# Optimization experiments

Measured on AMD Instinct MI355X. Metric: run time of the kernel, lower is better.

Reference implementation:

```python
import jax, jax.numpy as jnp
import numpy as np

V, D, H = 50000, 256, 4
HD = H * D            # concat head dim (TransformerConv concat=True)
HH, O = 256, 256      # invariant_hidden_dim, invariant_out_dim
B, N, E, L, A = 16, 1000, 4000, 64, 128
PAD = 0
SCALE = 1.0 / float(np.sqrt(D))


def emb_lookup(table, idx):
    # nn.Embedding with padding_idx: forward is a plain gather; grad at pad row is zeroed.
    rows = table[idx]
    return jnp.where((idx == PAD)[..., None], jax.lax.stop_gradient(rows), rows)


def transformer_conv(x, edge_index, ea, Wq, bq, Wk, bk, Wv, bv, We, Wskip, bskip):
    # PyG TransformerConv, heads=H, concat=True, root_weight=True, beta=False, dropout=0 (eval)
    n = x.shape[0]
    src, dst = edge_index[0], edge_index[1]
    q = (x @ Wq + bq).reshape(n, H, D)
    e = (ea @ We).reshape(-1, H, D)          # lin_edge (bias=False)
    k = (x @ Wk + bk).reshape(n, H, D)[src] + e
    v = (x @ Wv + bv).reshape(n, H, D)[src] + e
    alpha = (q[dst] * k).sum(-1) * SCALE      # [E,H]
    amax = jax.ops.segment_max(alpha, dst, num_segments=n)
    ex = jnp.exp(alpha - amax[dst])
    denom = jax.ops.segment_sum(ex, dst, num_segments=n)
    w = ex / denom[dst]                       # per-target-node softmax over incoming edges
    agg = jax.ops.segment_sum(v * w[..., None], dst, num_segments=n)
    return agg.reshape(n, HD) + x @ Wskip + bskip  # lin_skip on root


def mixed_embed(tok, node, graph_repr, emb):
    fixed = emb_lookup(emb, tok)
    flex = jnp.take_along_axis(graph_repr, node[..., None], axis=1)
    flex = jnp.where((node == PAD)[..., None], jax.lax.stop_gradient(flex), flex)
    return fixed + flex


def gru_last(xs, W_ih, W_hh, b_ih, b_hh):
    # torch nn.GRU, batch_first, 1 layer; only last hidden state is used
    gx = jnp.einsum('blh,gh->blg', xs, W_ih) + b_ih  # [B,L,3O]

    def step(h, g):
        gh = h @ W_hh.T + b_hh
        xr, xz, xn = jnp.split(g, 3, axis=-1)
        hr, hz, hn = jnp.split(gh, 3, axis=-1)
        r = jax.nn.sigmoid(xr + hr)
        z = jax.nn.sigmoid(xz + hz)
        c = jnp.tanh(xn + r * hn)
        return (1.0 - z) * c + z * h, None

    h0 = jnp.zeros((xs.shape[0], W_hh.shape[1]), xs.dtype)
    h_last, _ = jax.lax.scan(step, h0, jnp.swapaxes(gx, 0, 1))
    return h_last


def setup_inputs() -> dict:
    key = jax.random.key(0)
    ks = jax.random.split(key, 40)
    f = lambda i, shape, s=0.05: jax.random.normal(ks[i], shape, jnp.float32) * s
    ri = lambda i, shape, hi: jax.random.randint(ks[i], shape, 0, hi)
    return {
        'node_tokens': ri(0, (B, N), V),
        'edge_tokens': ri(1, (B, E), V),
        'edge_index': ri(2, (B, 2, E), N),
        'inv_token': ri(3, (B, L), V),
        'inv_node': ri(4, (B, L), N),
        'aa_token': ri(5, (B, A), V),
        'aa_node': ri(6, (B, A), N),
        'action_mask': jnp.ones((B, A), jnp.float32),
        'emb': f(7, (V, D), 0.02),
        'Wq': f(8, (D, HD)), 'bq': f(9, (HD,)),
        'Wk': f(10, (D, HD)), 'bk': f(11, (HD,)),
        'Wv': f(12, (D, HD)), 'bv': f(13, (HD,)),
        'We': f(14, (D, HD)),
        'Wskip': f(15, (D, HD)), 'bskip': f(16, (HD,)),
        'W1': f(17, (HD, D)), 'b1': f(18, (D,)),
        'Wp': f(19, (D, HH)), 'bp': f(20, (HH,)),
        'W_ih': f(21, (3 * O, HH)), 'W_hh': f(22, (3 * O, O)),
        'b_ih': f(23, (3 * O,)), 'b_hh': f(24, (3 * O,)),
        'Wab': f(25, (D, 1)), 'bab': f(26, (1,)),
        'Wap': f(27, (D, O)), 'bap': f(28, (O,)),
    }


def reference(node_tokens, edge_tokens, edge_index, inv_token, inv_node, aa_token, aa_node,
              action_mask, emb, Wq, bq, Wk, bk, Wv, bv, We, Wskip, bskip, W1, b1,
              Wp, bp, W_ih, W_hh, b_ih, b_hh, Wab, bab, Wap, bap):
    x = emb_lookup(emb, node_tokens)    # [B,N,D]
    ea = emb_lookup(emb, edge_tokens)   # [B,E,D]
    conv = jax.vmap(lambda xx, ei, ee: transformer_conv(
        xx, ei, ee, Wq, bq, Wk, bk, Wv, bv, We, Wskip, bskip))
    h = jax.nn.relu(conv(x, edge_index, ea))            # [B,N,HD]
    graph_repr = jax.nn.relu(h @ W1 + b1)               # [B,N,D]
    inv_h = jax.nn.relu(mixed_embed(inv_token, inv_node, graph_repr, emb) @ Wp + bp)
    inv = gru_last(inv_h, W_ih, W_hh, b_ih, b_hh)       # [B,O]
    aa_emb = mixed_embed(aa_token, aa_node, graph_repr, emb)  # [B,A,D]
    scores = jnp.einsum('bao,bo->ba', aa_emb @ Wap + bap, inv) + (aa_emb @ Wab + bab)[..., 0]
    inf_mask = jnp.maximum(jnp.log(action_mask), jnp.float32(np.finfo(np.float32).min))
    return scores + inf_mask
```

## Files before the change

kernel.cpp:

```cpp
#include <hip/hip_runtime.h>
#include <hip/hip_bf16.h>
#include <float.h>
#include <math.h>

typedef __hip_bfloat16 bf16;

#define B_ 16
#define N_ 1000
#define E_ 4000
#define L_ 64
#define A_ 128
#define D_ 256
#define H_ 4
#define HD_ 1024
#define SCALE_ 0.0625f

typedef __attribute__((ext_vector_type(8))) short short8;
typedef __attribute__((ext_vector_type(4))) float f32x4;

union U4S8 { uint4 u; short8 s; };

__device__ __forceinline__ unsigned short f2bf(float f) {
    bf16 h = __float2bfloat16(f);
    return *reinterpret_cast<unsigned short*>(&h);
}
__device__ __forceinline__ unsigned pack2(float a, float b) {
    return (unsigned)f2bf(a) | ((unsigned)f2bf(b) << 16);
}
__device__ __forceinline__ unsigned short rne1(float a) {
    unsigned ua = __float_as_uint(a);
    ua += 0x7fff + ((ua >> 16) & 1);
    return (unsigned short)(ua >> 16);
}
__device__ __forceinline__ float bflo(unsigned u) { return __uint_as_float(u << 16); }
__device__ __forceinline__ float bfhi(unsigned u) { return __uint_as_float(u & 0xffff0000u); }

#define LOG2E 1.4426950408889634f
__device__ __forceinline__ float fsigm(float x) {
    return __builtin_amdgcn_rcpf(1.f + __builtin_amdgcn_exp2f(-LOG2E * x));
}
__device__ __forceinline__ float ftanh(float x) {
    return 1.f - 2.f * __builtin_amdgcn_rcpf(1.f + __builtin_amdgcn_exp2f(2.f * LOG2E * x));
}

typedef const __attribute__((address_space(1))) unsigned int* gas_t;
typedef __attribute__((address_space(3))) unsigned int* las_t;
__device__ __forceinline__ void gld16(const void* g, void* l) {
    __builtin_amdgcn_global_load_lds((gas_t)g, (las_t)l, 16, 0, 0);
}

__global__ void convemb_kernel(const float* __restrict__ src, bf16* __restrict__ dst, long n4)
{
    long i = (long)blockIdx.x * 256 + threadIdx.x;
    if (i >= n4) return;
    float4 v = *(const float4*)(src + i * 4);
    *(uint2*)(dst + i * 4) = make_uint2(pack2(v.x, v.y), pack2(v.z, v.w));
}

__global__ void pack_all_kernel(const float* __restrict__ Wq, const float* __restrict__ Wk,
                                const float* __restrict__ Wv, const float* __restrict__ Wskip,
                                const float* __restrict__ We, const float* __restrict__ W1,
                                const float* __restrict__ Wp, const float* __restrict__ W_ih,
                                const float* __restrict__ Wap, const float* __restrict__ W_hh,
                                const float* __restrict__ bq, const float* __restrict__ bk,
                                const float* __restrict__ bv, const float* __restrict__ bskip,
                                unsigned* __restrict__ qkvsP, unsigned* __restrict__ WeP,
                                unsigned* __restrict__ W1P, unsigned* __restrict__ WpP,
                                unsigned* __restrict__ WihP, unsigned* __restrict__ WapP,
                                unsigned* __restrict__ WeTP,
                                short8* __restrict__ WhhP, float* __restrict__ bias4096)
{
    int i = blockIdx.x * 256 + threadIdx.x;
    if (i < 524288) {
        int k2 = i >> 12, n = i & 4095;
        const float* s = (n < 1024) ? Wq : (n < 2048) ? Wk : (n < 3072) ? Wv : Wskip;
        int col = n & 1023;
        qkvsP[i] = pack2(s[(long)(2 * k2) * 1024 + col], s[(long)(2 * k2 + 1) * 1024 + col]);
        return;
    }
    i -= 524288;
    if (i < 131072) {
        int k2 = i >> 10, n = i & 1023;
        WeP[i] = pack2(We[(long)(2 * k2) * 1024 + n], We[(long)(2 * k2 + 1) * 1024 + n]);
        return;
    }
    i -= 131072;
    if (i < 131072) {
        int k2 = i >> 8, n = i & 255;
        W1P[i] = pack2(W1[(long)(2 * k2) * 256 + n], W1[(long)(2 * k2 + 1) * 256 + n]);
        return;
    }
    i -= 131072;
    if (i < 32768) {
        int k2 = i >> 8, n = i & 255;
        WpP[i] = pack2(Wp[(long)(2 * k2) * 256 + n], Wp[(long)(2 * k2 + 1) * 256 + n]);
        return;
    }
    i -= 32768;
    if (i < 98304) {
        int k2 = i / 768, n = i % 768;
        WihP[i] = pack2(W_ih[(long)n * 256 + 2 * k2], W_ih[(long)n * 256 + 2 * k2 + 1]);
        return;
    }
    i -= 98304;
    if (i < 32768) {
        int k2 = i >> 8, n = i & 255;
        WapP[i] = pack2(Wap[(long)(2 * k2) * 256 + n], Wap[(long)(2 * k2 + 1) * 256 + n]);
        return;
    }
    i -= 32768;
    if (i < 131072) {
        int k2 = i >> 10, n = i & 1023;
        int d = n & 255, hb = n & ~255;
        WeTP[i] = pack2(We[(long)d * 1024 + hb + 2 * k2],
                        We[(long)d * 1024 + hb + 2 * k2 + 1]);
        return;
    }
    i -= 131072;
    if (i < 24576) {
        int lane = i & 63, tk = (i >> 6) & 7, tile = i >> 9;
        int n = tile * 16 + (lane & 15);
        const float* wp = W_hh + (long)n * 256 + tk * 32 + (lane >> 4) * 8;
        float4 w0 = *(const float4*)wp;
        float4 w1 = *(const float4*)(wp + 4);
        U4S8 u;
        u.u = make_uint4(pack2(w0.x, w0.y), pack2(w0.z, w0.w),
                         pack2(w1.x, w1.y), pack2(w1.z, w1.w));
        WhhP[i] = u.s;
        return;
    }
    i -= 24576;
    if (i < 4096) {
        int q = i >> 10, c = i & 1023;
        bias4096[i] = ((q == 0) ? bq : (q == 1) ? bk : (q == 2) ? bv : bskip)[c];
    }
}
#define PACK_ALL_TOT (524288 + 131072 + 131072 + 32768 + 98304 + 32768 + 131072 + 24576 + 4096)

#define TM 128
#define TN 128
#define TK 32
#define BSTR 132

template <typename CT>
__global__ __launch_bounds__(256)
void pgemm_kernel(const bf16* __restrict__ A, const int* __restrict__ arows,
                  const unsigned* __restrict__ Bp, const float* __restrict__ bias,
                  CT* __restrict__ C, int M, int K, int Nc, int relu_out,
                  long astride, int aoff, int colbase, int hslice, int addC, int outT)
{
    __shared__ short    As[TM * TK];
    __shared__ unsigned Bs[(TK / 2) * BSTR];

    const int tid  = threadIdx.x;
    const int lane = tid & 63;
    const int wave = tid >> 6;
    const int wm = wave >> 1, wn = wave & 1;
    const int quad = lane >> 4, c16 = lane & 15;
    const long row0 = (long)blockIdx.y * TM;
    const int  col0 = colbase + blockIdx.x * TN;
    const int  aoff2 = aoff + (hslice ? (col0 & ~255) : 0);

    {
    }
    const int r0 = wave * 32 + (lane >> 2);
    const int cseg = (lane & 3) * 8;
    long gr0 = row0 + r0;      if (gr0 > M - 1) gr0 = M - 1;
    long gr1 = row0 + r0 + 16; if (gr1 > M - 1) gr1 = M - 1;
    long ar0 = arows ? (long)arows[gr0] : gr0;
    long ar1 = arows ? (long)arows[gr1] : gr1;
    const short* Ag0 = (const short*)A + ar0 * astride + aoff2 + cseg;
    const short* Ag1 = (const short*)A + ar1 * astride + aoff2 + cseg;
    short* Ld0 = &As[wave * 1024];
    short* Ld1 = &As[wave * 1024 + 512];

    const int sn2 = tid & 63;
    const int skk = wave * 4;

    f32x4 acc[4][4];
    #pragma unroll
    for (int i = 0; i < 4; ++i)
        #pragma unroll
        for (int j = 0; j < 4; ++j)
            acc[i][j] = (f32x4){0.f, 0.f, 0.f, 0.f};

    for (int k0 = 0; k0 < K; k0 += TK) {
        gld16(Ag0 + k0, Ld0);
        gld16(Ag1 + k0, Ld1);
        #pragma unroll
        for (int i = 0; i < 4; ++i) {
            int kk2 = skk + i;
            *(uint2*)&Bs[kk2 * BSTR + sn2 * 2] =
                *(const uint2*)&Bp[(long)(k0 / 2 + kk2) * Nc + col0 + sn2 * 2];
        }
        __syncthreads();

        short8 af[4];
        U4S8   bfr[4];
        #pragma unroll
        for (int mi = 0; mi < 4; ++mi) {
            int m = wm * 64 + mi * 16 + c16;
            af[mi] = *(const short8*)&As[m * 32 + quad * 8];
        }
        #pragma unroll
        for (int ni = 0; ni < 4; ++ni) {
            int n = wn * 64 + ni * 16 + c16;
            uint4 u;
            u.x = Bs[(quad * 4 + 0) * BSTR + n];
            u.y = Bs[(quad * 4 + 1) * BSTR + n];
            u.z = Bs[(quad * 4 + 2) * BSTR + n];
            u.w = Bs[(quad * 4 + 3) * BSTR + n];
            bfr[ni].u = u;
        }
        #pragma unroll
        for (int mi = 0; mi < 4; ++mi)
            #pragma unroll
            for (int ni = 0; ni < 4; ++ni)
                acc[mi][ni] = __builtin_amdgcn_mfma_f32_16x16x32_bf16(
                    af[mi], bfr[ni].s, acc[mi][ni], 0, 0, 0);
        __syncthreads();
    }

    #pragma unroll
    for (int ni = 0; ni < 4; ++ni) {
        int col = col0 + wn * 64 + ni * 16 + c16;
        float bv = bias ? bias[col] : 0.f;
        #pragma unroll
        for (int mi = 0; mi < 4; ++mi) {
            long row = row0 + wm * 64 + mi * 16 + quad * 4;
            #pragma unroll
            for (int r = 0; r < 4; ++r) {
                if (row + r >= M) continue;
                float v = acc[mi][ni][r] + bv;
                if (addC) v += (float)C[(row + r) * Nc + col];
                if (relu_out) v = fmaxf(v, 0.f);
                if (outT) {
                    long rr = row + r;
                    int t = (int)(rr & 63), b = (int)(rr >> 6);
                    C[((long)t * Nc + col) * 16 + b] = (CT)v;
                } else {
                    C[(row + r) * Nc + col] = (CT)v;
                }
            }
        }
    }
}

__global__ void zero_int_kernel(int* __restrict__ p, int n)
{
    int i = blockIdx.x * 256 + threadIdx.x;
    if (i < n) p[i] = 0;
}

__global__ void count_kernel(const int* __restrict__ edge_index, int b0,
                             int* __restrict__ cnt, int cE)
{
    int i = blockIdx.x * 256 + threadIdx.x;
    if (i >= cE) return;
    int bl = i / E_, ei = i % E_;
    int dst = edge_index[(long)(b0 + bl) * 2 * E_ + E_ + ei];
    atomicAdd(&cnt[bl * N_ + dst], 1);
}

__global__ __launch_bounds__(1024)
void scan_kernel(const int* __restrict__ cnt, int* __restrict__ row_start,
                 int* __restrict__ cursor)
{
    int bl = blockIdx.x;
    int tid = threadIdx.x;
    __shared__ int s[1024];
    int v = (tid < N_) ? cnt[bl * N_ + tid] : 0;
    s[tid] = v;
    __syncthreads();
    for (int off = 1; off < 1024; off <<= 1) {
        int t = (tid >= off) ? s[tid - off] : 0;
        __syncthreads();
        s[tid] += t;
        __syncthreads();
    }
    if (tid < N_) {
        int excl = s[tid] - v;
        row_start[bl * N_ + tid] = excl;
        cursor[bl * N_ + tid] = excl;
    }
}

__global__ void scatter_kernel(const int* __restrict__ edge_index, int b0,
                               int* __restrict__ cursor, int* __restrict__ elist, int cE)
{
    int i = blockIdx.x * 256 + threadIdx.x;
    if (i >= cE) return;
    int bl = i / E_, ei = i % E_;
    int dst = edge_index[(long)(b0 + bl) * 2 * E_ + E_ + ei];
    int pos = atomicAdd(&cursor[bl * N_ + dst], 1);
    elist[bl * E_ + pos] = ei;
}

__device__ __forceinline__ float d2(unsigned a, unsigned b)
{
    return bflo(a) * bflo(b) + bfhi(a) * bfhi(b);
}

__global__ void attn_kernel(const bf16* __restrict__ qkvs, const bf16* __restrict__ qWb,
                            const bf16* __restrict__ embh,
                            const int* __restrict__ edge_tokens, const int* __restrict__ edge_index,
                            const int* __restrict__ row_start, const int* __restrict__ cnt,
                            const int* __restrict__ elist, int b0,
                            bf16* __restrict__ aggb, bf16* __restrict__ xsumb)
{
    int base = blockIdx.x;
    int bl = base / N_;
    int tid = threadIdx.x;
    int l = tid & 63;
    int j0 = tid * 4;
    int jx = l * 4;

    uint2 qq = *(const uint2*)(qkvs + (long)base * 4096 + j0);
    uint2 ww = *(const uint2*)(qWb + (long)base * 1024 + j0);

    int start = row_start[base];
    int deg = cnt[base];
    const int* el = elist + (long)bl * E_;
    const int* srcp = edge_index + (long)(b0 + bl) * 2 * E_;
    const int* tokp = edge_tokens + (long)(b0 + bl) * E_;

    float denom = 0.f;
    float v0 = 0.f, v1 = 0.f, v2 = 0.f, v3 = 0.f;
    float x0 = 0.f, x1 = 0.f, x2 = 0.f, x3 = 0.f;

    for (int t = 0; t < deg; ++t) {
        int ei = el[start + t];
        int src = srcp[ei];
        int tok = tokp[ei];
        const bf16* srow = qkvs + (long)(bl * N_ + src) * 4096;
        uint2 kk = *(const uint2*)(srow + 1024 + j0);
        uint2 vv = *(const uint2*)(srow + 2048 + j0);
        uint2 xx = *(const uint2*)(embh + (long)tok * 256 + jx);

        float s = d2(qq.x, kk.x) + d2(qq.y, kk.y) + d2(ww.x, xx.x) + d2(ww.y, xx.y);
        s += __shfl_xor(s, 32);
        s += __shfl_xor(s, 16);
        s += __shfl_xor(s, 8);
        s += __shfl_xor(s, 4);
        s += __shfl_xor(s, 2);
        s += __shfl_xor(s, 1);
        float ex = __builtin_amdgcn_exp2f(s * (SCALE_ * LOG2E));

        denom += ex;
        v0 += ex * bflo(vv.x); v1 += ex * bfhi(vv.x);
        v2 += ex * bflo(vv.y); v3 += ex * bfhi(vv.y);
        x0 += ex * bflo(xx.x); x1 += ex * bfhi(xx.x);
        x2 += ex * bflo(xx.y); x3 += ex * bfhi(xx.y);
    }

    float invd = (deg > 0) ? 1.f / denom : 0.f;
    uint2 sk = *(const uint2*)(qkvs + (long)base * 4096 + 3072 + j0);
    unsigned o0 = pack2(bflo(sk.x) + v0 * invd, bfhi(sk.x) + v1 * invd);
    unsigned o1 = pack2(bflo(sk.y) + v2 * invd, bfhi(sk.y) + v3 * invd);
    *(uint2*)(aggb + (long)base * HD_ + j0) = make_uint2(o0, o1);
    *(uint2*)(xsumb + (long)base * HD_ + j0) =
        make_uint2(pack2(x0 * invd, x1 * invd), pack2(x2 * invd, x3 * invd));
}

__global__ void mixed2_kernel(const bf16* __restrict__ embh,
                              const int* __restrict__ inv_token, const int* __restrict__ inv_node,
                              const int* __restrict__ aa_token, const int* __restrict__ aa_node,
                              const float* __restrict__ graph_repr,
                              bf16* __restrict__ mixed_inv, bf16* __restrict__ aa_emb)
{
    int r = blockIdx.x;
    int d = threadIdx.x;
    if (r < B_ * L_) {
        int b = r / L_;
        float v = (float)embh[(long)inv_token[r] * D_ + d] +
                  graph_repr[((long)b * N_ + inv_node[r]) * D_ + d];
        mixed_inv[(long)r * D_ + d] = __float2bfloat16(v);
    } else {
        int r2 = r - B_ * L_;
        int b = r2 / A_;
        float v = (float)embh[(long)aa_token[r2] * D_ + d] +
                  graph_repr[((long)b * N_ + aa_node[r2]) * D_ + d];
        aa_emb[(long)r2 * D_ + d] = __float2bfloat16(v);
    }
}

__global__ __launch_bounds__(1024)
void gru_kernel(const bf16* __restrict__ gxT, const short8* __restrict__ WhhP,
                const float* __restrict__ b_hh, float* __restrict__ inv_out)
{
    __shared__ short hB[2][16 * 264];

    const int tid = threadIdx.x;
    const int lane = tid & 63;
    const int wave = tid >> 6;
    const int quad = lane >> 4, c16 = lane & 15;
    const int n0 = wave * 16 + c16;

    for (int i = tid; i < 2 * 16 * 264; i += 1024) ((short*)hB)[i] = 0;

    short8 wfr[8], wfz[8], wfn[8];
    #pragma unroll
    for (int tk = 0; tk < 8; ++tk) {
        wfr[tk] = WhhP[((0 * 16 + wave) * 8 + tk) * 64 + lane];
        wfz[tk] = WhhP[((1 * 16 + wave) * 8 + tk) * 64 + lane];
        wfn[tk] = WhhP[((2 * 16 + wave) * 8 + tk) * 64 + lane];
    }
    float bhr = b_hh[0 * 256 + n0];
    float bhz = b_hh[1 * 256 + n0];
    float bhn = b_hh[2 * 256 + n0];

    float myh0 = 0.f, myh1 = 0.f, myh2 = 0.f, myh3 = 0.f;

    const short* gbr = (const short*)gxT + (long)(0 * 256 + n0) * 16 + quad * 4;
    const short* gbz = gbr + 256 * 16;
    const short* gbn = gbr + 512 * 16;

    uint2 pxr = *(const uint2*)gbr;
    uint2 pxz = *(const uint2*)gbz;
    uint2 pxn = *(const uint2*)gbn;

    __syncthreads();

    int p = 0;
    for (int t = 0; t < L_; ++t) {
        uint2 xr2 = pxr, xz2 = pxz, xn2 = pxn;
        long noff = (long)((t + 1 < L_) ? t + 1 : t) * 12288;
        pxr = *(const uint2*)(gbr + noff);
        pxz = *(const uint2*)(gbz + noff);
        pxn = *(const uint2*)(gbn + noff);

        f32x4 ar = (f32x4){bhr, bhr, bhr, bhr};
        f32x4 az = (f32x4){bhz, bhz, bhz, bhz};
        f32x4 an = (f32x4){bhn, bhn, bhn, bhn};
        const short* hp = &hB[p][0];
        #pragma unroll
        for (int tk = 0; tk < 8; ++tk) {
            short8 a = *(const short8*)&hp[c16 * 264 + tk * 32 + quad * 8];
            ar = __builtin_amdgcn_mfma_f32_16x16x32_bf16(a, wfr[tk], ar, 0, 0, 0);
            az = __builtin_amdgcn_mfma_f32_16x16x32_bf16(a, wfz[tk], az, 0, 0, 0);
            an = __builtin_amdgcn_mfma_f32_16x16x32_bf16(a, wfn[tk], an, 0, 0, 0);
        }

        float xr[4] = {bflo(xr2.x), bfhi(xr2.x), bflo(xr2.y), bfhi(xr2.y)};
        float xz[4] = {bflo(xz2.x), bfhi(xz2.x), bflo(xz2.y), bfhi(xz2.y)};
        float xn[4] = {bflo(xn2.x), bfhi(xn2.x), bflo(xn2.y), bfhi(xn2.y)};
        float hold[4] = {myh0, myh1, myh2, myh3};
        float hn[4];
        short* hw = &hB[p ^ 1][0];
        #pragma unroll
        for (int r = 0; r < 4; ++r) {
            float rr = fsigm(xr[r] + ar[r]);
            float zz = fsigm(xz[r] + az[r]);
            float cc = ftanh(xn[r] + rr * an[r]);
            hn[r] = (1.f - zz) * cc + zz * hold[r];
            hw[(quad * 4 + r) * 264 + n0] = (short)rne1(hn[r]);
        }
        myh0 = hn[0]; myh1 = hn[1]; myh2 = hn[2]; myh3 = hn[3];
        p ^= 1;
        __syncthreads();
    }

    inv_out[(long)(quad * 4 + 0) * 256 + n0] = myh0;
    inv_out[(long)(quad * 4 + 1) * 256 + n0] = myh1;
    inv_out[(long)(quad * 4 + 2) * 256 + n0] = myh2;
    inv_out[(long)(quad * 4 + 3) * 256 + n0] = myh3;
}

__global__ void score_kernel(const float* __restrict__ aa_p, const bf16* __restrict__ aa_emb,
                             const float* __restrict__ inv, const float* __restrict__ Wab,
                             const float* __restrict__ bab, const float* __restrict__ mask,
                             float* __restrict__ out)
{
    int r = blockIdx.x * 4 + (threadIdx.x >> 6);
    int l = threadIdx.x & 63;
    int b = r / A_;
    float s = 0.f;
    for (int d = l; d < D_; d += 64)
        s += aa_p[(long)r * D_ + d] * inv[(long)b * D_ + d] +
             (float)aa_emb[(long)r * D_ + d] * Wab[d];
    #pragma unroll
    for (int off = 32; off; off >>= 1) s += __shfl_down(s, off);
    if (l == 0) {
        float lm = logf(mask[r]);
        const float MN = -3.4028234663852886e38f;
        if (!(lm >= MN)) lm = MN;
        out[r] = s + bab[0] + lm;
    }
}

static inline size_t align256(size_t x) { return (x + 255) & ~(size_t)255; }

template <typename CT>
static void launch_pgemm(const bf16* A, const int* arows, const unsigned* Bp,
                         const float* bias, CT* C, int M, int K, int Nc, int relu,
                         long astride, int aoff, int colbase, int hslice, int addC,
                         int outT, int ncols, hipStream_t s)
{
    dim3 grid(ncols / TN, (M + TM - 1) / TM);
    pgemm_kernel<CT><<<grid, 256, 0, s>>>(A, arows, Bp, bias, C, M, K, Nc, relu,
                                          astride, aoff, colbase, hslice, addC, outT);
}

extern "C" void kernel_launch(void* const* d_in, const int* in_sizes, int n_in,
                              void* d_out, int out_size, void* d_ws, size_t ws_size,
                              hipStream_t stream)
{
    const int* node_tokens = (const int*)d_in[0];
    const int* edge_tokens = (const int*)d_in[1];
    const int* edge_index  = (const int*)d_in[2];
    const int* inv_token   = (const int*)d_in[3];
    const int* inv_node    = (const int*)d_in[4];
    const int* aa_token    = (const int*)d_in[5];
    const int* aa_node     = (const int*)d_in[6];
    const float* action_mask = (const float*)d_in[7];
    const float* emb   = (const float*)d_in[8];
    const float* Wq    = (const float*)d_in[9];
    const float* bq    = (const float*)d_in[10];
    const float* Wk    = (const float*)d_in[11];
    const float* bk    = (const float*)d_in[12];
    const float* Wv    = (const float*)d_in[13];
    const float* bv    = (const float*)d_in[14];
    const float* We    = (const float*)d_in[15];
    const float* Wskip = (const float*)d_in[16];
    const float* bskip = (const float*)d_in[17];
    const float* W1    = (const float*)d_in[18];
    const float* b1    = (const float*)d_in[19];
    const float* Wp    = (const float*)d_in[20];
    const float* bp    = (const float*)d_in[21];
    const float* W_ih  = (const float*)d_in[22];
    const float* W_hh  = (const float*)d_in[23];
    const float* b_ih  = (const float*)d_in[24];
    const float* b_hh  = (const float*)d_in[25];
    const float* Wab   = (const float*)d_in[26];
    const float* bab   = (const float*)d_in[27];
    const float* Wap   = (const float*)d_in[28];
    const float* bap   = (const float*)d_in[29];
    (void)in_sizes; (void)n_in; (void)out_size;

    char* base = (char*)d_ws;
    size_t off = 0;
    auto alloc = [&](size_t bytes) -> char* {
        char* p = base + off;
        off = align256(off + bytes);
        return p;
    };

    const long VD = 50000L * 256;
    bf16*  embh       = (bf16*)alloc(VD * 2);
    float* graph_repr = (float*)alloc((size_t)B_ * N_ * D_ * 4);
    bf16*  mixed_inv  = (bf16*)alloc((size_t)B_ * L_ * D_ * 2);
    bf16*  inv_h      = (bf16*)alloc((size_t)B_ * L_ * D_ * 2);
    bf16*  gxT        = (bf16*)alloc((size_t)B_ * L_ * 768 * 2);
    float* inv_out    = (float*)alloc((size_t)B_ * 256 * 4);
    bf16*  aa_emb     = (bf16*)alloc((size_t)B_ * A_ * D_ * 2);
    float* aa_p       = (float*)alloc((size_t)B_ * A_ * 256 * 4);
    unsigned* qkvsP   = (unsigned*)alloc((size_t)128 * 4096 * 4);
    unsigned* WeP     = (unsigned*)alloc((size_t)128 * 1024 * 4);
    unsigned* W1P     = (unsigned*)alloc((size_t)512 * 256 * 4);
    unsigned* WpP     = (unsigned*)alloc((size_t)128 * 256 * 4);
    unsigned* WihP    = (unsigned*)alloc((size_t)128 * 768 * 4);
    unsigned* WapP    = (unsigned*)alloc((size_t)128 * 256 * 4);
    unsigned* WeTP    = (unsigned*)alloc((size_t)128 * 1024 * 4);
    short8* WhhP      = (short8*)alloc((size_t)24576 * 16);
    float* bias4096   = (float*)alloc(4096 * 4);
    size_t persist = off;

    int c = 16;
    while (c > 1) {
        size_t cN = (size_t)c * N_, cEs = (size_t)c * E_;
        size_t chunk = align256(cN * 4096 * 2)
                     + align256(cN * HD_ * 2)
                     + align256(cN * HD_ * 2)
                     + align256(cN * HD_ * 2)
                     + 3 * align256(cN * 4)
                     + align256(cEs * 4);
        if (persist + chunk <= ws_size) break;
        c >>= 1;
    }
    int cN = c * N_, cE = c * E_;

    bf16*  qkvs  = (bf16*)alloc((size_t)cN * 4096 * 2);
    bf16*  qWb   = (bf16*)alloc((size_t)cN * HD_ * 2);
    bf16*  aggb  = (bf16*)alloc((size_t)cN * HD_ * 2);
    bf16*  xsumb = (bf16*)alloc((size_t)cN * HD_ * 2);
    int*   cnt   = (int*)alloc((size_t)cN * 4);
    int*   rstart= (int*)alloc((size_t)cN * 4);
    int*   cursor= (int*)alloc((size_t)cN * 4);
    int*   elist = (int*)alloc((size_t)cE * 4);

    convemb_kernel<<<(int)((VD / 4 + 255) / 256), 256, 0, stream>>>(emb, embh, VD / 4);
    pack_all_kernel<<<(PACK_ALL_TOT + 255) / 256, 256, 0, stream>>>(
        Wq, Wk, Wv, Wskip, We, W1, Wp, W_ih, Wap, W_hh, bq, bk, bv, bskip,
        qkvsP, WeP, W1P, WpP, WihP, WapP, WeTP, WhhP, bias4096);

    for (int b0 = 0; b0 < B_; b0 += c) {
        zero_int_kernel<<<(cN + 255) / 256, 256, 0, stream>>>(cnt, cN);
        count_kernel<<<(cE + 255) / 256, 256, 0, stream>>>(edge_index, b0, cnt, cE);
        scan_kernel<<<c, 1024, 0, stream>>>(cnt, rstart, cursor);
        scatter_kernel<<<(cE + 255) / 256, 256, 0, stream>>>(edge_index, b0, cursor,
                                                             elist, cE);
        launch_pgemm<bf16>(embh, node_tokens + (long)b0 * N_, qkvsP, bias4096, qkvs,
                           cN, D_, 4096, 0, 256, 0, 0, 0, 0, 0, 4096, stream);
        launch_pgemm<bf16>(qkvs, nullptr, WeTP, nullptr, qWb,
                           cN, 256, 1024, 0, 4096, 0, 0, 1, 0, 0, 1024, stream);
        attn_kernel<<<cN, 256, 0, stream>>>(qkvs, qWb, embh, edge_tokens, edge_index,
                                            rstart, cnt, elist, b0, aggb, xsumb);
        launch_pgemm<bf16>(xsumb, nullptr, WeP, nullptr, aggb,
                           cN, 256, 1024, 1, 1024, 0, 0, 1, 1, 0, 1024, stream);
        launch_pgemm<float>(aggb, nullptr, W1P, b1,
                            graph_repr + (long)b0 * N_ * D_,
                            cN, HD_, D_, 1, 1024, 0, 0, 0, 0, 0, 256, stream);
    }

    mixed2_kernel<<<B_ * L_ + B_ * A_, 256, 0, stream>>>(embh, inv_token, inv_node,
                                                         aa_token, aa_node, graph_repr,
                                                         mixed_inv, aa_emb);
    launch_pgemm<bf16>(mixed_inv, nullptr, WpP, bp, inv_h,
                       B_ * L_, D_, 256, 1, 256, 0, 0, 0, 0, 0, 256, stream);
    launch_pgemm<bf16>(inv_h, nullptr, WihP, b_ih, gxT,
                       B_ * L_, 256, 768, 0, 256, 0, 0, 0, 0, 1, 768, stream);
    gru_kernel<<<1, 1024, 0, stream>>>(gxT, WhhP, b_hh, inv_out);

    launch_pgemm<float>(aa_emb, nullptr, WapP, bap, aa_p,
                        B_ * A_, D_, 256, 0, 256, 0, 0, 0, 0, 0, 256, stream);
    score_kernel<<<(B_ * A_) / 4, 256, 0, stream>>>(aa_p, aa_emb, inv_out, Wab, bab,
                                                    action_mask, (float*)d_out);
}
```

Baseline: 849.2 us.

## Prefetch edges in attention, bf16 graph_repr, split GRU batch, fold Wap into inv

The attention loop now prefetches the next edge's key, value and embedding rows while the current edge is processed. graph_repr is stored as bf16 instead of fp32. The GRU runs on four blocks, each handling four batch rows, instead of one block handling all sixteen. The aa_emb @ Wap GEMM is replaced by a per-batch vector u = Wap·inv + Wab, so scoring becomes a single dot product per action. Together these aim to hide gather latency, halve graph_repr traffic, parallelise the serial GRU, and drop a GEMM, at the cost of bf16 rounding in graph_repr and a reordered summation in the score.

```diff
diff --git a/kernel.cpp b/kernel.cpp
--- a/kernel.cpp
+++ b/kernel.cpp
@@ -161,8 +161,6 @@
     const int  col0 = colbase + blockIdx.x * TN;
     const int  aoff2 = aoff + (hslice ? (col0 & ~255) : 0);
 
-    {
-    }
     const int r0 = wave * 32 + (lane >> 2);
     const int cseg = (lane & 3) * 8;
     long gr0 = row0 + r0;      if (gr0 > M - 1) gr0 = M - 1;
@@ -328,16 +326,28 @@
     float v0 = 0.f, v1 = 0.f, v2 = 0.f, v3 = 0.f;
     float x0 = 0.f, x1 = 0.f, x2 = 0.f, x3 = 0.f;
 
+    uint2 kk = make_uint2(0, 0), vv = make_uint2(0, 0), xx = make_uint2(0, 0);
+    if (deg > 0) {
+        int e0 = el[start];
+        int s0 = srcp[e0], t0 = tokp[e0];
+        const bf16* srow = qkvs + (long)(bl * N_ + s0) * 4096;
+        kk = *(const uint2*)(srow + 1024 + j0);
+        vv = *(const uint2*)(srow + 2048 + j0);
+        xx = *(const uint2*)(embh + (long)t0 * 256 + jx);
+    }
+
     for (int t = 0; t < deg; ++t) {
-        int ei = el[start + t];
-        int src = srcp[ei];
-        int tok = tokp[ei];
-        const bf16* srow = qkvs + (long)(bl * N_ + src) * 4096;
-        uint2 kk = *(const uint2*)(srow + 1024 + j0);
-        uint2 vv = *(const uint2*)(srow + 2048 + j0);
-        uint2 xx = *(const uint2*)(embh + (long)tok * 256 + jx);
-
-        float s = d2(qq.x, kk.x) + d2(qq.y, kk.y) + d2(ww.x, xx.x) + d2(ww.y, xx.y);
+        uint2 ck = kk, cv = vv, cx = xx;
+        if (t + 1 < deg) {
+            int ne = el[start + t + 1];
+            int ns = srcp[ne], nt = tokp[ne];
+            const bf16* srow = qkvs + (long)(bl * N_ + ns) * 4096;
+            kk = *(const uint2*)(srow + 1024 + j0);
+            vv = *(const uint2*)(srow + 2048 + j0);
+            xx = *(const uint2*)(embh + (long)nt * 256 + jx);
+        }
+
+        float s = d2(qq.x, ck.x) + d2(qq.y, ck.y) + d2(ww.x, cx.x) + d2(ww.y, cx.y);
         s += __shfl_xor(s, 32);
         s += __shfl_xor(s, 16);
         s += __shfl_xor(s, 8);
@@ -347,10 +357,10 @@
         float ex = __builtin_amdgcn_exp2f(s * (SCALE_ * LOG2E));
 
         denom += ex;
-        v0 += ex * bflo(vv.x); v1 += ex * bfhi(vv.x);
-        v2 += ex * bflo(vv.y); v3 += ex * bfhi(vv.y);
-        x0 += ex * bflo(xx.x); x1 += ex * bfhi(xx.x);
-        x2 += ex * bflo(xx.y); x3 += ex * bfhi(xx.y);
+        v0 += ex * bflo(cv.x); v1 += ex * bfhi(cv.x);
+        v2 += ex * bflo(cv.y); v3 += ex * bfhi(cv.y);
+        x0 += ex * bflo(cx.x); x1 += ex * bfhi(cx.x);
+        x2 += ex * bflo(cx.y); x3 += ex * bfhi(cx.y);
     }
 
     float invd = (deg > 0) ? 1.f / denom : 0.f;
@@ -365,7 +375,7 @@
 __global__ void mixed2_kernel(const bf16* __restrict__ embh,
                               const int* __restrict__ inv_token, const int* __restrict__ inv_node,
                               const int* __restrict__ aa_token, const int* __restrict__ aa_node,
-                              const float* __restrict__ graph_repr,
+                              const bf16* __restrict__ graph_repr,
                               bf16* __restrict__ mixed_inv, bf16* __restrict__ aa_emb)
 {
     int r = blockIdx.x;
@@ -373,13 +383,13 @@
     if (r < B_ * L_) {
         int b = r / L_;
         float v = (float)embh[(long)inv_token[r] * D_ + d] +
-                  graph_repr[((long)b * N_ + inv_node[r]) * D_ + d];
+                  (float)graph_repr[((long)b * N_ + inv_node[r]) * D_ + d];
         mixed_inv[(long)r * D_ + d] = __float2bfloat16(v);
     } else {
         int r2 = r - B_ * L_;
         int b = r2 / A_;
         float v = (float)embh[(long)aa_token[r2] * D_ + d] +
-                  graph_repr[((long)b * N_ + aa_node[r2]) * D_ + d];
+                  (float)graph_repr[((long)b * N_ + aa_node[r2]) * D_ + d];
         aa_emb[(long)r2 * D_ + d] = __float2bfloat16(v);
     }
 }
@@ -395,6 +405,7 @@
     const int wave = tid >> 6;
     const int quad = lane >> 4, c16 = lane & 15;
     const int n0 = wave * 16 + c16;
+    const int bb = blockIdx.x * 4 + quad;
 
     for (int i = tid; i < 2 * 16 * 264; i += 1024) ((short*)hB)[i] = 0;
 
@@ -409,25 +420,23 @@
     float bhz = b_hh[1 * 256 + n0];
     float bhn = b_hh[2 * 256 + n0];
 
-    float myh0 = 0.f, myh1 = 0.f, myh2 = 0.f, myh3 = 0.f;
-
-    const short* gbr = (const short*)gxT + (long)(0 * 256 + n0) * 16 + quad * 4;
-    const short* gbz = gbr + 256 * 16;
-    const short* gbn = gbr + 512 * 16;
-
-    uint2 pxr = *(const uint2*)gbr;
-    uint2 pxz = *(const uint2*)gbz;
-    uint2 pxn = *(const uint2*)gbn;
+    float myh = 0.f;
+
+    const unsigned short* g_r = (const unsigned short*)gxT + (long)n0 * 16 + bb;
+    const unsigned short* g_z = g_r + 256 * 16;
+    const unsigned short* g_n = g_r + 512 * 16;
+
+    unsigned short pr = g_r[0], pz = g_z[0], pn = g_n[0];
 
     __syncthreads();
 
     int p = 0;
     for (int t = 0; t < L_; ++t) {
-        uint2 xr2 = pxr, xz2 = pxz, xn2 = pxn;
+        float xr = __uint_as_float((unsigned)pr << 16);
+        float xz = __uint_as_float((unsigned)pz << 16);
+        float xn = __uint_as_float((unsigned)pn << 16);
         long noff = (long)((t + 1 < L_) ? t + 1 : t) * 12288;
-        pxr = *(const uint2*)(gbr + noff);
-        pxz = *(const uint2*)(gbz + noff);
-        pxn = *(const uint2*)(gbn + noff);
+        pr = g_r[noff]; pz = g_z[noff]; pn = g_n[noff];
 
         f32x4 ar = (f32x4){bhr, bhr, bhr, bhr};
         f32x4 az = (f32x4){bhz, bhz, bhz, bhz};
@@ -441,34 +450,41 @@
             an = __builtin_amdgcn_mfma_f32_16x16x32_bf16(a, wfn[tk], an, 0, 0, 0);
         }
 
-        float xr[4] = {bflo(xr2.x), bfhi(xr2.x), bflo(xr2.y), bfhi(xr2.y)};
-        float xz[4] = {bflo(xz2.x), bfhi(xz2.x), bflo(xz2.y), bfhi(xz2.y)};
-        float xn[4] = {bflo(xn2.x), bfhi(xn2.x), bflo(xn2.y), bfhi(xn2.y)};
-        float hold[4] = {myh0, myh1, myh2, myh3};
-        float hn[4];
-        short* hw = &hB[p ^ 1][0];
-        #pragma unroll
-        for (int r = 0; r < 4; ++r) {
-            float rr = fsigm(xr[r] + ar[r]);
-            float zz = fsigm(xz[r] + az[r]);
-            float cc = ftanh(xn[r] + rr * an[r]);
-            hn[r] = (1.f - zz) * cc + zz * hold[r];
-            hw[(quad * 4 + r) * 264 + n0] = (short)rne1(hn[r]);
-        }
-        myh0 = hn[0]; myh1 = hn[1]; myh2 = hn[2]; myh3 = hn[3];
+        float rr = fsigm(xr + ar[0]);
+        float zz = fsigm(xz + az[0]);
+        float cc = ftanh(xn + rr * an[0]);
+        myh = (1.f - zz) * cc + zz * myh;
+        hB[p ^ 1][(quad * 4) * 264 + n0] = (short)rne1(myh);
         p ^= 1;
         __syncthreads();
     }
 
-    inv_out[(long)(quad * 4 + 0) * 256 + n0] = myh0;
-    inv_out[(long)(quad * 4 + 1) * 256 + n0] = myh1;
-    inv_out[(long)(quad * 4 + 2) * 256 + n0] = myh2;
-    inv_out[(long)(quad * 4 + 3) * 256 + n0] = myh3;
-}
-
-__global__ void score_kernel(const float* __restrict__ aa_p, const bf16* __restrict__ aa_emb,
-                             const float* __restrict__ inv, const float* __restrict__ Wab,
-                             const float* __restrict__ bab, const float* __restrict__ mask,
+    inv_out[(long)bb * 256 + n0] = myh;
+}
+
+__global__ void uprep_kernel(const float* __restrict__ Wap, const float* __restrict__ Wab,
+                             const float* __restrict__ bap, const float* __restrict__ bab,
+                             const float* __restrict__ inv, float* __restrict__ u,
+                             float* __restrict__ s0)
+{
+    int b = blockIdx.x, d = threadIdx.x;
+    __shared__ float iv[256];
+    iv[d] = inv[(long)b * 256 + d];
+    __syncthreads();
+    float s = Wab[d];
+    const float* wr = Wap + (long)d * 256;
+    #pragma unroll 8
+    for (int o = 0; o < 256; ++o) s += wr[o] * iv[o];
+    u[(long)b * 256 + d] = s;
+    if (d == 0) {
+        float t = bab[0];
+        for (int o = 0; o < 256; ++o) t += bap[o] * iv[o];
+        s0[b] = t;
+    }
+}
+
+__global__ void score_kernel(const bf16* __restrict__ aa_emb, const float* __restrict__ u,
+                             const float* __restrict__ s0, const float* __restrict__ mask,
                              float* __restrict__ out)
 {
     int r = blockIdx.x * 4 + (threadIdx.x >> 6);
@@ -476,15 +492,14 @@
     int b = r / A_;
     float s = 0.f;
     for (int d = l; d < D_; d += 64)
-        s += aa_p[(long)r * D_ + d] * inv[(long)b * D_ + d] +
-             (float)aa_emb[(long)r * D_ + d] * Wab[d];
+        s += (float)aa_emb[(long)r * D_ + d] * u[(long)b * D_ + d];
     #pragma unroll
     for (int off = 32; off; off >>= 1) s += __shfl_down(s, off);
     if (l == 0) {
         float lm = logf(mask[r]);
         const float MN = -3.4028234663852886e38f;
         if (!(lm >= MN)) lm = MN;
-        out[r] = s + bab[0] + lm;
+        out[r] = s + s0[b] + lm;
     }
 }
 
@@ -547,13 +562,14 @@
 
     const long VD = 50000L * 256;
     bf16*  embh       = (bf16*)alloc(VD * 2);
-    float* graph_repr = (float*)alloc((size_t)B_ * N_ * D_ * 4);
+    bf16*  graph_repr = (bf16*)alloc((size_t)B_ * N_ * D_ * 2);
     bf16*  mixed_inv  = (bf16*)alloc((size_t)B_ * L_ * D_ * 2);
     bf16*  inv_h      = (bf16*)alloc((size_t)B_ * L_ * D_ * 2);
     bf16*  gxT        = (bf16*)alloc((size_t)B_ * L_ * 768 * 2);
     float* inv_out    = (float*)alloc((size_t)B_ * 256 * 4);
     bf16*  aa_emb     = (bf16*)alloc((size_t)B_ * A_ * D_ * 2);
-    float* aa_p       = (float*)alloc((size_t)B_ * A_ * 256 * 4);
+    float* ubuf       = (float*)alloc((size_t)B_ * 256 * 4);
+    float* s0buf      = (float*)alloc((size_t)B_ * 4);
     unsigned* qkvsP   = (unsigned*)alloc((size_t)128 * 4096 * 4);
     unsigned* WeP     = (unsigned*)alloc((size_t)128 * 1024 * 4);
     unsigned* W1P     = (unsigned*)alloc((size_t)512 * 256 * 4);
@@ -607,9 +623,9 @@
                                             rstart, cnt, elist, b0, aggb, xsumb);
         launch_pgemm<bf16>(xsumb, nullptr, WeP, nullptr, aggb,
                            cN, 256, 1024, 1, 1024, 0, 0, 1, 1, 0, 1024, stream);
-        launch_pgemm<float>(aggb, nullptr, W1P, b1,
-                            graph_repr + (long)b0 * N_ * D_,
-                            cN, HD_, D_, 1, 1024, 0, 0, 0, 0, 0, 256, stream);
+        launch_pgemm<bf16>(aggb, nullptr, W1P, b1,
+                           graph_repr + (long)b0 * N_ * D_,
+                           cN, HD_, D_, 1, 1024, 0, 0, 0, 0, 0, 256, stream);
     }
 
     mixed2_kernel<<<B_ * L_ + B_ * A_, 256, 0, stream>>>(embh, inv_token, inv_node,
@@ -619,10 +635,9 @@
                        B_ * L_, D_, 256, 1, 256, 0, 0, 0, 0, 0, 256, stream);
     launch_pgemm<bf16>(inv_h, nullptr, WihP, b_ih, gxT,
                        B_ * L_, 256, 768, 0, 256, 0, 0, 0, 0, 1, 768, stream);
-    gru_kernel<<<1, 1024, 0, stream>>>(gxT, WhhP, b_hh, inv_out);
-
-    launch_pgemm<float>(aa_emb, nullptr, WapP, bap, aa_p,
-                        B_ * A_, D_, 256, 0, 256, 0, 0, 0, 0, 0, 256, stream);
-    score_kernel<<<(B_ * A_) / 4, 256, 0, stream>>>(aa_p, aa_emb, inv_out, Wab, bab,
+    gru_kernel<<<4, 1024, 0, stream>>>(gxT, WhhP, b_hh, inv_out);
+
+    uprep_kernel<<<B_, 256, 0, stream>>>(Wap, Wab, bap, bab, inv_out, ubuf, s0buf);
+    score_kernel<<<(B_ * A_) / 4, 256, 0, stream>>>(aa_emb, ubuf, s0buf,
                                                     action_mask, (float*)d_out);
 }
```

Measured after the change: 798.3 us. -6.0%, faster.
